# Kernel optimization log

Hardware: AMD Instinct MI355X
Metric: run time of the kernel (lower is better)

## Reference

```python
import jax, jax.numpy as jnp
import numpy as np

B, S, H = 1, 2048, 4096
NQ, NKV, D = 32, 8, 128
N_REP = NQ // NKV
SCALE = 1.0 / np.sqrt(D)
SOFTCAP = 30.0
EPS = 1e-5


def _rotate_half(x):
    x1, x2 = jnp.split(x, 2, axis=-1)
    return jnp.concatenate([-x2, x1], axis=-1)


def _rms_norm(x, w, eps=EPS):
    xf = x.astype(jnp.float32)
    norm = xf * jax.lax.rsqrt(jnp.mean(xf * xf, axis=-1, keepdims=True) + eps)
    return (w * norm).astype(x.dtype)


def setup_inputs() -> dict:
    key = jax.random.key(0)
    ks = jax.random.split(key, 8)
    hidden_states = jax.random.normal(ks[0], (B, S, H), dtype=jnp.float32)
    # causal additive mask
    causal = jnp.tril(jnp.ones((S, S), dtype=bool))
    attention_mask = jnp.where(causal, 0.0, -1e9)[None, None].astype(jnp.float32)
    # RoPE cache
    inv_freq = 1.0 / (10000.0 ** (np.arange(0, D, 2, dtype=np.float32) / D))
    t = np.arange(S, dtype=np.float32)
    freqs = np.outer(t, inv_freq)                      # (S, D/2)
    emb = np.concatenate([freqs, freqs], axis=-1)      # (S, D)
    cos = jnp.asarray(np.cos(emb))[None, None]         # (1,1,S,D)
    sin = jnp.asarray(np.sin(emb))[None, None]
    # params
    std = 0.02
    wq = jax.random.normal(ks[1], (NQ * D, H), dtype=jnp.float32) * std
    wk = jax.random.normal(ks[2], (NKV * D, H), dtype=jnp.float32) * std
    wv = jax.random.normal(ks[3], (NKV * D, H), dtype=jnp.float32) * std
    wo = jax.random.normal(ks[4], (H, NQ * D), dtype=jnp.float32) * std
    pre_norm_w = jnp.ones((H,), dtype=jnp.float32)
    q_norm_w = jnp.ones((D,), dtype=jnp.float32)
    k_norm_w = jnp.ones((D,), dtype=jnp.float32)
    return {
        "hidden_states": hidden_states, "attention_mask": attention_mask,
        "cos": cos, "sin": sin, "pre_norm_w": pre_norm_w,
        "wq": wq, "wk": wk, "wv": wv, "wo": wo,
        "q_norm_w": q_norm_w, "k_norm_w": k_norm_w,
    }


def reference(hidden_states, attention_mask, cos, sin, pre_norm_w,
              wq, wk, wv, wo, q_norm_w, k_norm_w):
    residual = hidden_states
    h = _rms_norm(hidden_states, pre_norm_w)
    bsz, seq_len, _ = h.shape
    # projections -> (b, heads, s, d)
    q = jnp.einsum('bsh,eh->bse', h, wq).reshape(bsz, seq_len, NQ, D).transpose(0, 2, 1, 3)
    k = jnp.einsum('bsh,eh->bse', h, wk).reshape(bsz, seq_len, NKV, D).transpose(0, 2, 1, 3)
    v = jnp.einsum('bsh,eh->bse', h, wv).reshape(bsz, seq_len, NKV, D).transpose(0, 2, 1, 3)
    # QK RMSNorm over head_dim
    q = _rms_norm(q, q_norm_w)
    k = _rms_norm(k, k_norm_w)
    # RoPE (full head_dim)
    q = q * cos + _rotate_half(q) * sin
    k = k * cos + _rotate_half(k) * sin
    # GQA: repeat kv heads
    k_exp = jnp.repeat(k, N_REP, axis=1)  # (b, NQ, s, d)
    v_exp = jnp.repeat(v, N_REP, axis=1)
    scores = jnp.einsum('bhqd,bhkd->bhqk', q, k_exp) * SCALE
    scores = SOFTCAP * jnp.tanh(scores / SOFTCAP)
    scores = scores + attention_mask
    probs = jax.nn.softmax(scores.astype(jnp.float32), axis=-1).astype(q.dtype)
    attn = jnp.einsum('bhqk,bhkd->bhqd', probs, v_exp)
    attn = attn.transpose(0, 2, 1, 3).reshape(bsz, seq_len, NQ * D)
    out = jnp.einsum('bse,he->bsh', attn, wo)
    return residual + out
```

## Files before the change

kernel.cpp:

```cpp
#include <hip/hip_runtime.h>
#include <cstdint>

typedef __bf16 bf16;
typedef __bf16 bf16x8 __attribute__((ext_vector_type(8)));
typedef __bf16 bf16x4 __attribute__((ext_vector_type(4)));
typedef float  f32x4  __attribute__((ext_vector_type(4)));

#define SEQ  2048
#define HID  4096
#define DH   128
#define NQH  32
#define NKVH 8
#define RSCALE 0.08838834764831845f
#define SOFTCAP 30.0f
#define L2E 1.4426950408889634f

__device__ __forceinline__ void gl2lds16(const void* g, void* l) {
  __builtin_amdgcn_global_load_lds(
      (const __attribute__((address_space(1))) unsigned int*)g,
      (__attribute__((address_space(3))) unsigned int*)l, 16, 0, 0);
}

__global__ void cvt_kernel(const float* __restrict__ in, bf16* __restrict__ out, int n4) {
  const int stride = gridDim.x * blockDim.x;
  for (int i = blockIdx.x * blockDim.x + threadIdx.x; i < n4; i += stride) {
    const float4 v = ((const float4*)in)[i];
    bf16x4 o = { (bf16)v.x, (bf16)v.y, (bf16)v.z, (bf16)v.w };
    *(bf16x4*)(out + (size_t)i * 4) = o;
  }
}

__global__ void rmsnorm_kernel(const float* __restrict__ x, const float* __restrict__ w,
                               bf16* __restrict__ out) {
  const int s = blockIdx.x;
  const float* xr = x + (size_t)s * HID;
  float4 v[4];
  float ss = 0.f;
#pragma unroll
  for (int j = 0; j < 4; ++j) {
    v[j] = ((const float4*)xr)[threadIdx.x + j * 256];
    ss += v[j].x * v[j].x + v[j].y * v[j].y + v[j].z * v[j].z + v[j].w * v[j].w;
  }
#pragma unroll
  for (int m = 1; m < 64; m <<= 1) ss += __shfl_xor(ss, m);
  __shared__ float red[4];
  if ((threadIdx.x & 63) == 0) red[threadIdx.x >> 6] = ss;
  __syncthreads();
  const float rn = rsqrtf((red[0] + red[1] + red[2] + red[3]) * (1.f / HID) + 1e-5f);
  bf16* orow = out + (size_t)s * HID;
#pragma unroll
  for (int j = 0; j < 4; ++j) {
    const int idx = (threadIdx.x + j * 256) * 4;
    const float4 wv = ((const float4*)w)[threadIdx.x + j * 256];
    bf16x4 o = { (bf16)(v[j].x * rn * wv.x), (bf16)(v[j].y * rn * wv.y),
                 (bf16)(v[j].z * rn * wv.z), (bf16)(v[j].w * rn * wv.w) };
    *(bf16x4*)(orow + idx) = o;
  }
}

template<bool FINAL>
__global__ __launch_bounds__(256, 3)
void gemm_bt(const bf16* __restrict__ A, const bf16* __restrict__ B,
             bf16* __restrict__ Cb, float* __restrict__ Cf,
             const float* __restrict__ resid, int M, int N, int K)
{
  __shared__ bf16 As[128 * 64];
  __shared__ bf16 Bs[128 * 64];
  const int tid  = threadIdx.x;
  const int lane = tid & 63;
  const int wave = tid >> 6;
  const int wm = wave >> 1, wn = wave & 1;

  const int gx = gridDim.x;
  const int nwg = gx * gridDim.y;
  int lin = blockIdx.x + gx * blockIdx.y;
  lin = (lin & 7) * (nwg >> 3) + (lin >> 3);
  const int m0 = (lin / gx) * 128, n0 = (lin % gx) * 128;

  f32x4 acc[4][4] = {};

  for (int kt = 0; kt < K; kt += 64) {
#pragma unroll
    for (int i = 0; i < 4; ++i) {
      const int c = wave * 4 + i;
      const int row = c * 8 + (lane >> 3);
      const int col8 = (lane & 7) ^ (row & 7);
      gl2lds16(A + (size_t)(m0 + row) * K + kt + col8 * 8, As + c * 512);
      gl2lds16(B + (size_t)(n0 + row) * K + kt + col8 * 8, Bs + c * 512);
    }
    __syncthreads();
#pragma unroll
    for (int ks = 0; ks < 2; ++ks) {
      bf16x8 af[4], bfv[4];
#pragma unroll
      for (int mi = 0; mi < 4; ++mi) {
        const int row = wm * 64 + mi * 16 + (lane & 15);
        const int slot = (ks * 4 + (lane >> 4)) ^ (row & 7);
        af[mi] = *(const bf16x8*)(As + row * 64 + slot * 8);
      }
#pragma unroll
      for (int ni = 0; ni < 4; ++ni) {
        const int row = wn * 64 + ni * 16 + (lane & 15);
        const int slot = (ks * 4 + (lane >> 4)) ^ (row & 7);
        bfv[ni] = *(const bf16x8*)(Bs + row * 64 + slot * 8);
      }
#pragma unroll
      for (int mi = 0; mi < 4; ++mi)
#pragma unroll
        for (int ni = 0; ni < 4; ++ni)
          acc[mi][ni] = __builtin_amdgcn_mfma_f32_16x16x32_bf16(af[mi], bfv[ni], acc[mi][ni], 0, 0, 0);
    }
    __syncthreads();
  }

#pragma unroll
  for (int mi = 0; mi < 4; ++mi) {
#pragma unroll
    for (int i = 0; i < 4; ++i) {
      const int m = m0 + wm * 64 + mi * 16 + (lane >> 4) * 4 + i;
#pragma unroll
      for (int ni = 0; ni < 4; ++ni) {
        const int n = n0 + wn * 64 + ni * 16 + (lane & 15);
        const float v = acc[mi][ni][i];
        if constexpr (FINAL) {
          Cf[(size_t)m * N + n] = v + resid[(size_t)m * N + n];
        } else {
          Cb[(size_t)m * N + n] = (bf16)v;
        }
      }
    }
  }
}

__global__ void qkrope_kernel(const bf16* __restrict__ qpj, const bf16* __restrict__ kpj,
                              const float* __restrict__ qw, const float* __restrict__ kw,
                              const float* __restrict__ cs, const float* __restrict__ sn,
                              bf16* __restrict__ qr, bf16* __restrict__ kr)
{
  const int w = blockIdx.x * 4 + (threadIdx.x >> 6);
  const int lane = threadIdx.x & 63;
  const int s = w / (NQH + NKVH);
  const int hh = w % (NQH + NKVH);
  const bf16* src; bf16* dst; const float* nw;
  if (hh < NQH) {
    src = qpj + (size_t)s * (NQH * DH) + hh * DH;
    dst = qr + ((size_t)hh * SEQ + s) * DH;
    nw = qw;
  } else {
    const int h2 = hh - NQH;
    src = kpj + (size_t)s * 2048 + h2 * DH;
    dst = kr + ((size_t)h2 * SEQ + s) * DH;
    nw = kw;
  }
  const float x0 = (float)src[lane], x1 = (float)src[lane + 64];
  float ss = x0 * x0 + x1 * x1;
#pragma unroll
  for (int m = 1; m < 64; m <<= 1) ss += __shfl_xor(ss, m);
  const float rn = rsqrtf(ss * (1.f / DH) + 1e-5f);
  const float n0 = x0 * rn * nw[lane], n1 = x1 * rn * nw[lane + 64];
  const float c0 = cs[s * DH + lane],      s0 = sn[s * DH + lane];
  const float c1 = cs[s * DH + lane + 64], s1 = sn[s * DH + lane + 64];
  dst[lane]      = (bf16)(n0 * c0 - n1 * s0);
  dst[lane + 64] = (bf16)(n1 * c1 + n0 * s1);
}

__global__ void vtrans_kernel(const bf16* __restrict__ vsrc, bf16* __restrict__ vt)
{
  __shared__ bf16 tbuf[64][33];
  const int s0 = blockIdx.x * 64;
  const int d0 = blockIdx.y * 32;
  const int h  = blockIdx.z;
  const int tid = threadIdx.x;
  {
    const int col = tid & 31, r0 = tid >> 5;
    for (int r = r0; r < 64; r += 8)
      tbuf[r][col] = vsrc[(size_t)(s0 + r) * 2048 + 1024 + h * DH + d0 + col];
  }
  __syncthreads();
  {
    const int sc = tid & 63, dr0 = tid >> 6;
    for (int d = dr0; d < 32; d += 4)
      vt[((size_t)h * DH + d0 + d) * SEQ + s0 + sc] = tbuf[sc][d];
  }
}

__global__ __launch_bounds__(256, 2)
void attn_kernel(const bf16* __restrict__ Q, const bf16* __restrict__ Kr,
                 const bf16* __restrict__ Vt, bf16* __restrict__ Oa)
{
  __shared__ bf16 Ks[2][64 * 128];
  __shared__ bf16 Vs[2][128 * 64];
  __shared__ bf16 Ps[4][32 * 64];

  const int tid = threadIdx.x, lane = tid & 63, wave = tid >> 6;

  const int lin  = blockIdx.x + 16 * blockIdx.y;
  const int slot = lin >> 8, idx = lin & 255;
  const int bx   = slot ? (15 - (idx & 15)) : (idx & 15);
  const int head = (slot << 4) | (idx >> 4);
  const int kvh  = head >> 2;
  const int q0   = bx * 128;
  const int wq0  = q0 + wave * 32;

  const bf16* Qh = Q  + (size_t)head * SEQ * DH;
  const bf16* Kh = Kr + (size_t)kvh * SEQ * DH;
  const bf16* Vh = Vt + (size_t)kvh * DH * SEQ;

  bf16x8 qf[2][4];
#pragma unroll
  for (int mt = 0; mt < 2; ++mt)
#pragma unroll
    for (int kc = 0; kc < 4; ++kc) {
      const int r = wq0 + mt * 16 + (lane & 15);
      qf[mt][kc] = *(const bf16x8*)(Qh + (size_t)r * DH + kc * 32 + (lane >> 4) * 8);
    }

  float lsum[2][4] = {};
  f32x4 o_acc[2][8] = {};

  const int ntiles = q0 / 64 + 2;

  auto stage = [&](int t, int b) {
    const int kv0 = t * 64;
    bf16* Kd = &Ks[b][0];
    bf16* Vd = &Vs[b][0];
#pragma unroll
    for (int i2 = 0; i2 < 4; ++i2) {
      const int c = wave * 4 + i2;
      {
        const int row = c * 4 + (lane >> 4);
        const int col8 = (lane & 15) ^ (row & 15);
        gl2lds16(Kh + (size_t)(kv0 + row) * DH + col8 * 8, Kd + c * 512);
      }
      {
        const int row = c * 8 + (lane >> 3);
        const int col8 = (lane & 7) ^ (row & 7);
        gl2lds16(Vh + (size_t)row * SEQ + kv0 + col8 * 8, Vd + c * 512);
      }
    }
  };

  stage(0, 0);
  __syncthreads();

  const float ZS = RSCALE / SOFTCAP;
  const float A1 = RSCALE * L2E;
  const float B3 = -(ZS * ZS) * (1.f / 3.f);
  const float B5 = (2.f / 15.f) * (ZS * ZS) * (ZS * ZS);
  const float C  = SOFTCAP * L2E;

  for (int t = 0; t < ntiles; ++t) {
    const int cur = t & 1;
    if (t + 1 < ntiles) stage(t + 1, cur ^ 1);
    const int kv0 = t * 64;
    const bf16* Kb = &Ks[cur][0];
    const bf16* Vb = &Vs[cur][0];

    if (kv0 <= wq0 + 31) {
      f32x4 sc[2][4] = {};
      __builtin_amdgcn_s_setprio(1);
#pragma unroll
      for (int ks = 0; ks < 4; ++ks) {
        bf16x8 kf[4];
#pragma unroll
        for (int nt = 0; nt < 4; ++nt) {
          const int row = nt * 16 + (lane & 15);
          const int sl = (ks * 4 + (lane >> 4)) ^ (row & 15);
          kf[nt] = *(const bf16x8*)(Kb + row * 128 + sl * 8);
        }
#pragma unroll
        for (int mt = 0; mt < 2; ++mt)
#pragma unroll
          for (int nt = 0; nt < 4; ++nt)
            sc[mt][nt] = __builtin_amdgcn_mfma_f32_16x16x32_bf16(qf[mt][ks], kf[nt], sc[mt][nt], 0, 0, 0);
      }
      __builtin_amdgcn_s_setprio(0);

      if (kv0 + 63 <= wq0) {
#pragma unroll
        for (int mt = 0; mt < 2; ++mt)
#pragma unroll
          for (int i = 0; i < 4; ++i)
#pragma unroll
            for (int nt = 0; nt < 4; ++nt) {
              const float s = sc[mt][nt][i];
              const float w = s * s;
              const float poly = fmaf(fmaf(B5, w, B3), w, 1.f);
              const float p = __builtin_amdgcn_exp2f(fmaf(s * poly, A1, -C));
              sc[mt][nt][i] = p;
              lsum[mt][i] += p;
            }
      } else {
#pragma unroll
        for (int mt = 0; mt < 2; ++mt)
#pragma unroll
          for (int i = 0; i < 4; ++i) {
            const int qrow = wq0 + mt * 16 + (lane >> 4) * 4 + i;
#pragma unroll
            for (int nt = 0; nt < 4; ++nt) {
              const int col = kv0 + nt * 16 + (lane & 15);
              const float s = sc[mt][nt][i];
              const float w = s * s;
              const float poly = fmaf(fmaf(B5, w, B3), w, 1.f);
              float p = __builtin_amdgcn_exp2f(fmaf(s * poly, A1, -C));
              if (col > qrow) p = 0.f;
              sc[mt][nt][i] = p;
              lsum[mt][i] += p;
            }
          }
      }

#pragma unroll
      for (int mt = 0; mt < 2; ++mt)
#pragma unroll
        for (int nt = 0; nt < 4; ++nt)
#pragma unroll
          for (int i = 0; i < 4; ++i) {
            const int r = mt * 16 + (lane >> 4) * 4 + i;
            const int colb = nt * 16 + (lane & 15);
            const int sl = (colb >> 3) ^ (r & 7);
            Ps[wave][r * 64 + sl * 8 + (colb & 7)] = (bf16)sc[mt][nt][i];
          }
      asm volatile("s_waitcnt lgkmcnt(0)" ::: "memory");
      __builtin_amdgcn_sched_barrier(0);

      __builtin_amdgcn_s_setprio(1);
#pragma unroll
      for (int ks2 = 0; ks2 < 2; ++ks2) {
        bf16x8 pf[2];
#pragma unroll
        for (int mt = 0; mt < 2; ++mt) {
          const int r = mt * 16 + (lane & 15);
          const int sl = (ks2 * 4 + (lane >> 4)) ^ (r & 7);
          pf[mt] = *(const bf16x8*)(&Ps[wave][r * 64 + sl * 8]);
        }
#pragma unroll
        for (int nt = 0; nt < 8; ++nt) {
          const int row = nt * 16 + (lane & 15);
          const int sl = (ks2 * 4 + (lane >> 4)) ^ (row & 7);
          const bf16x8 vf = *(const bf16x8*)(Vb + row * 64 + sl * 8);
          o_acc[0][nt] = __builtin_amdgcn_mfma_f32_16x16x32_bf16(pf[0], vf, o_acc[0][nt], 0, 0, 0);
          o_acc[1][nt] = __builtin_amdgcn_mfma_f32_16x16x32_bf16(pf[1], vf, o_acc[1][nt], 0, 0, 0);
        }
      }
      __builtin_amdgcn_s_setprio(0);
    }
    __syncthreads();
  }

#pragma unroll
  for (int mt = 0; mt < 2; ++mt)
#pragma unroll
    for (int i = 0; i < 4; ++i) {
      float l = lsum[mt][i];
#pragma unroll
      for (int m = 1; m < 16; m <<= 1) l += __shfl_xor(l, m);
      const int qrow = wq0 + mt * 16 + (lane >> 4) * 4 + i;
      const float inv_l = 1.f / l;
#pragma unroll
      for (int nt = 0; nt < 8; ++nt) {
        const int d = nt * 16 + (lane & 15);
        Oa[(size_t)qrow * HID + head * DH + d] = (bf16)(o_acc[mt][nt][i] * inv_l);
      }
    }
}

extern "C" void kernel_launch(void* const* d_in, const int* in_sizes, int n_in,
                              void* d_out, int out_size, void* d_ws, size_t ws_size,
                              hipStream_t stream)
{
  const float* hidden = (const float*)d_in[0];
  const float* cosb   = (const float*)d_in[2];
  const float* sinb   = (const float*)d_in[3];
  const float* prew   = (const float*)d_in[4];
  const float* wq     = (const float*)d_in[5];
  const float* wk     = (const float*)d_in[6];
  const float* wv     = (const float*)d_in[7];
  const float* wo     = (const float*)d_in[8];
  const float* qnw    = (const float*)d_in[9];
  const float* knw    = (const float*)d_in[10];
  float* outp = (float*)d_out;
  char* ws = (char*)d_ws;

  bf16* wqb  = (bf16*)(ws + 0);
  bf16* wkvb = (bf16*)(ws + 33554432);
  bf16* kvpj = (bf16*)(ws + 50331648);
  bf16* hb   = (bf16*)(ws + 58720256);
  bf16* qpj  = (bf16*)(ws + 75497472);
  bf16* kr   = (bf16*)(ws + 92274688);
  bf16* vt   = (bf16*)(ws + 96468992);

  cvt_kernel<<<2048, 256, 0, stream>>>(wq, wqb, (NQH * DH) * HID / 4);
  cvt_kernel<<<1024, 256, 0, stream>>>(wk, wkvb, (NKVH * DH) * HID / 4);
  cvt_kernel<<<1024, 256, 0, stream>>>(wv, wkvb + (size_t)(NKVH * DH) * HID, (NKVH * DH) * HID / 4);
  rmsnorm_kernel<<<SEQ, 256, 0, stream>>>(hidden, prew, hb);

  gemm_bt<false><<<dim3(32, 16), 256, 0, stream>>>(hb, wqb,  qpj,  nullptr, nullptr, SEQ, 4096, 4096);
  gemm_bt<false><<<dim3(16, 16), 256, 0, stream>>>(hb, wkvb, kvpj, nullptr, nullptr, SEQ, 2048, 4096);

  qkrope_kernel<<<SEQ * (NQH + NKVH) / 4, 256, 0, stream>>>(qpj, kvpj, qnw, knw, cosb, sinb, hb, kr);
  vtrans_kernel<<<dim3(32, 4, 8), 256, 0, stream>>>(kvpj, vt);
  cvt_kernel<<<2048, 256, 0, stream>>>(wo, wqb, (NQH * DH) * HID / 4);

  attn_kernel<<<dim3(16, 32), 256, 0, stream>>>(hb, kr, vt, qpj);

  gemm_bt<true><<<dim3(32, 16), 256, 0, stream>>>(qpj, wqb, nullptr, outp, hidden, SEQ, 4096, 4096);
}
```

Baseline: 376.2 us.

## Fuse QKV projection GEMMs and add triple-buffered 8-wave 128x256 GEMM pipeline

Merges the Q and KV projection weights into one contiguous QKV matrix so a single GEMM produces all projections, and retargets the rope and V-transpose kernels to the fused layout. Replaces the 4-wave 128x128 GEMM with an 8-wave 128x256 tile kernel that uses 144KB of dynamic LDS for triple buffering. Loads are prefetched two tiles ahead, split across the two k-substeps, with explicit waitcnt, barriers and setprio around the MFMAs. The goal is to overlap global loads with compute and cut launch and tail overhead. In exchange it runs only one workgroup per CU and depends on fragile hand-placed synchronisation.

```diff
diff --git a/kernel.cpp b/kernel.cpp
--- a/kernel.cpp
+++ b/kernel.cpp
@@ -11,6 +11,7 @@
 #define DH   128
 #define NQH  32
 #define NKVH 8
+#define NTOT 6144
 #define RSCALE 0.08838834764831845f
 #define SOFTCAP 30.0f
 #define L2E 1.4426950408889634f
@@ -59,36 +60,68 @@
 }
 
 template<bool FINAL>
-__global__ __launch_bounds__(256, 3)
-void gemm_bt(const bf16* __restrict__ A, const bf16* __restrict__ B,
-             bf16* __restrict__ Cb, float* __restrict__ Cf,
-             const float* __restrict__ resid, int M, int N, int K)
+__global__ __launch_bounds__(512, 1)
+void gemm8(const bf16* __restrict__ A, const bf16* __restrict__ B,
+           bf16* __restrict__ Cb, float* __restrict__ Cf,
+           const float* __restrict__ resid, int M, int N, int K)
 {
-  __shared__ bf16 As[128 * 64];
-  __shared__ bf16 Bs[128 * 64];
+  extern __shared__ char smem[];
   const int tid  = threadIdx.x;
   const int lane = tid & 63;
   const int wave = tid >> 6;
-  const int wm = wave >> 1, wn = wave & 1;
+  const int wm = wave >> 2, wn = wave & 3;
 
   const int gx = gridDim.x;
   const int nwg = gx * gridDim.y;
   int lin = blockIdx.x + gx * blockIdx.y;
   lin = (lin & 7) * (nwg >> 3) + (lin >> 3);
-  const int m0 = (lin / gx) * 128, n0 = (lin % gx) * 128;
+  const int m0 = (lin / gx) * 128;
+  const int n0 = (lin % gx) * 256;
+
+  auto Abuf = [&](int b) -> bf16* { return (bf16*)(smem + b * 49152); };
+  auto Bbuf = [&](int b) -> bf16* { return (bf16*)(smem + b * 49152 + 16384); };
+
+  auto stage_half = [&](int kt, int b, int h) {
+    if (h == 0) {
+#pragma unroll
+      for (int i = 0; i < 2; ++i) {
+        const int c = wave * 2 + i;
+        const int row = c * 8 + (lane >> 3);
+        const int col8 = (lane & 7) ^ (row & 7);
+        gl2lds16(A + (size_t)(m0 + row) * K + kt + col8 * 8, Abuf(b) + c * 512);
+      }
+      {
+        const int c = wave * 4;
+        const int row = c * 8 + (lane >> 3);
+        const int col8 = (lane & 7) ^ (row & 7);
+        gl2lds16(B + (size_t)(n0 + row) * K + kt + col8 * 8, Bbuf(b) + c * 512);
+      }
+    } else {
+#pragma unroll
+      for (int i = 1; i < 4; ++i) {
+        const int c = wave * 4 + i;
+        const int row = c * 8 + (lane >> 3);
+        const int col8 = (lane & 7) ^ (row & 7);
+        gl2lds16(B + (size_t)(n0 + row) * K + kt + col8 * 8, Bbuf(b) + c * 512);
+      }
+    }
+  };
 
   f32x4 acc[4][4] = {};
-
-  for (int kt = 0; kt < K; kt += 64) {
-#pragma unroll
-    for (int i = 0; i < 4; ++i) {
-      const int c = wave * 4 + i;
-      const int row = c * 8 + (lane >> 3);
-      const int col8 = (lane & 7) ^ (row & 7);
-      gl2lds16(A + (size_t)(m0 + row) * K + kt + col8 * 8, As + c * 512);
-      gl2lds16(B + (size_t)(n0 + row) * K + kt + col8 * 8, Bs + c * 512);
-    }
-    __syncthreads();
+  const int nt = K / 64;
+
+  stage_half(0, 0, 0);  stage_half(0, 0, 1);
+  stage_half(64, 1, 0); stage_half(64, 1, 1);
+  asm volatile("s_waitcnt vmcnt(6)" ::: "memory");
+  __builtin_amdgcn_s_barrier();
+
+  for (int t = 0; t < nt; ++t) {
+    const int cur = t % 3;
+    const bf16* Ab = Abuf(cur);
+    const bf16* Bb = Bbuf(cur);
+    const int nxt = (t + 2) % 3;
+    const bool pf = (t + 2) < nt;
+
 #pragma unroll
     for (int ks = 0; ks < 2; ++ks) {
       bf16x8 af[4], bfv[4];
@@ -96,21 +129,33 @@
       for (int mi = 0; mi < 4; ++mi) {
         const int row = wm * 64 + mi * 16 + (lane & 15);
         const int slot = (ks * 4 + (lane >> 4)) ^ (row & 7);
-        af[mi] = *(const bf16x8*)(As + row * 64 + slot * 8);
+        af[mi] = *(const bf16x8*)(Ab + row * 64 + slot * 8);
       }
 #pragma unroll
       for (int ni = 0; ni < 4; ++ni) {
         const int row = wn * 64 + ni * 16 + (lane & 15);
         const int slot = (ks * 4 + (lane >> 4)) ^ (row & 7);
-        bfv[ni] = *(const bf16x8*)(Bs + row * 64 + slot * 8);
-      }
+        bfv[ni] = *(const bf16x8*)(Bb + row * 64 + slot * 8);
+      }
+      if (pf) stage_half((t + 2) * 64, nxt, ks);
+
+      __builtin_amdgcn_s_barrier();
+      asm volatile("s_waitcnt lgkmcnt(0)" ::: "memory");
+      __builtin_amdgcn_sched_barrier(0);
+      __builtin_amdgcn_s_setprio(1);
 #pragma unroll
       for (int mi = 0; mi < 4; ++mi)
 #pragma unroll
         for (int ni = 0; ni < 4; ++ni)
           acc[mi][ni] = __builtin_amdgcn_mfma_f32_16x16x32_bf16(af[mi], bfv[ni], acc[mi][ni], 0, 0, 0);
-    }
-    __syncthreads();
+      __builtin_amdgcn_s_setprio(0);
+
+      if (ks == 1) {
+        if (pf)                asm volatile("s_waitcnt vmcnt(6)" ::: "memory");
+        else if (t + 1 < nt)   asm volatile("s_waitcnt vmcnt(0)" ::: "memory");
+      }
+      __builtin_amdgcn_s_barrier();
+    }
   }
 
 #pragma unroll
@@ -132,7 +177,7 @@
   }
 }
 
-__global__ void qkrope_kernel(const bf16* __restrict__ qpj, const bf16* __restrict__ kpj,
+__global__ void qkrope_kernel(const bf16* __restrict__ qkv,
                               const float* __restrict__ qw, const float* __restrict__ kw,
                               const float* __restrict__ cs, const float* __restrict__ sn,
                               bf16* __restrict__ qr, bf16* __restrict__ kr)
@@ -143,12 +188,12 @@
   const int hh = w % (NQH + NKVH);
   const bf16* src; bf16* dst; const float* nw;
   if (hh < NQH) {
-    src = qpj + (size_t)s * (NQH * DH) + hh * DH;
+    src = qkv + (size_t)s * NTOT + hh * DH;
     dst = qr + ((size_t)hh * SEQ + s) * DH;
     nw = qw;
   } else {
     const int h2 = hh - NQH;
-    src = kpj + (size_t)s * 2048 + h2 * DH;
+    src = qkv + (size_t)s * NTOT + 4096 + h2 * DH;
     dst = kr + ((size_t)h2 * SEQ + s) * DH;
     nw = kw;
   }
@@ -164,7 +209,7 @@
   dst[lane + 64] = (bf16)(n1 * c1 + n0 * s1);
 }
 
-__global__ void vtrans_kernel(const bf16* __restrict__ vsrc, bf16* __restrict__ vt)
+__global__ void vtrans_kernel(const bf16* __restrict__ qkv, bf16* __restrict__ vt)
 {
   __shared__ bf16 tbuf[64][33];
   const int s0 = blockIdx.x * 64;
@@ -174,7 +219,7 @@
   {
     const int col = tid & 31, r0 = tid >> 5;
     for (int r = r0; r < 64; r += 8)
-      tbuf[r][col] = vsrc[(size_t)(s0 + r) * 2048 + 1024 + h * DH + d0 + col];
+      tbuf[r][col] = qkv[(size_t)(s0 + r) * NTOT + 5120 + h * DH + d0 + col];
   }
   __syncthreads();
   {
@@ -382,27 +427,28 @@
   float* outp = (float*)d_out;
   char* ws = (char*)d_ws;
 
-  bf16* wqb  = (bf16*)(ws + 0);
-  bf16* wkvb = (bf16*)(ws + 33554432);
-  bf16* kvpj = (bf16*)(ws + 50331648);
-  bf16* hb   = (bf16*)(ws + 58720256);
-  bf16* qpj  = (bf16*)(ws + 75497472);
+  bf16* wqkv = (bf16*)(ws + 0);
+  bf16* hb   = (bf16*)(ws + 50331648);
+  bf16* qkvp = (bf16*)(ws + 67108864);
   bf16* kr   = (bf16*)(ws + 92274688);
   bf16* vt   = (bf16*)(ws + 96468992);
-
-  cvt_kernel<<<2048, 256, 0, stream>>>(wq, wqb, (NQH * DH) * HID / 4);
-  cvt_kernel<<<1024, 256, 0, stream>>>(wk, wkvb, (NKVH * DH) * HID / 4);
-  cvt_kernel<<<1024, 256, 0, stream>>>(wv, wkvb + (size_t)(NKVH * DH) * HID, (NKVH * DH) * HID / 4);
+  bf16* wob  = wqkv;
+
+  cvt_kernel<<<2048, 256, 0, stream>>>(wq, wqkv, 4096 * HID / 4);
+  cvt_kernel<<<1024, 256, 0, stream>>>(wk, wqkv + (size_t)4096 * HID, 1024 * HID / 4);
+  cvt_kernel<<<1024, 256, 0, stream>>>(wv, wqkv + (size_t)5120 * HID, 1024 * HID / 4);
   rmsnorm_kernel<<<SEQ, 256, 0, stream>>>(hidden, prew, hb);
 
-  gemm_bt<false><<<dim3(32, 16), 256, 0, stream>>>(hb, wqb,  qpj,  nullptr, nullptr, SEQ, 4096, 4096);
-  gemm_bt<false><<<dim3(16, 16), 256, 0, stream>>>(hb, wkvb, kvpj, nullptr, nullptr, SEQ, 2048, 4096);
-
-  qkrope_kernel<<<SEQ * (NQH + NKVH) / 4, 256, 0, stream>>>(qpj, kvpj, qnw, knw, cosb, sinb, hb, kr);
-  vtrans_kernel<<<dim3(32, 4, 8), 256, 0, stream>>>(kvpj, vt);
-  cvt_kernel<<<2048, 256, 0, stream>>>(wo, wqb, (NQH * DH) * HID / 4);
-
-  attn_kernel<<<dim3(16, 32), 256, 0, stream>>>(hb, kr, vt, qpj);
-
-  gemm_bt<true><<<dim3(32, 16), 256, 0, stream>>>(qpj, wqb, nullptr, outp, hidden, SEQ, 4096, 4096);
-}
+  gemm8<false><<<dim3(NTOT / 256, SEQ / 128), 512, 147456, stream>>>(
+      hb, wqkv, qkvp, nullptr, nullptr, SEQ, NTOT, HID);
+
+  cvt_kernel<<<2048, 256, 0, stream>>>(wo, wob, HID * HID / 4);
+
+  qkrope_kernel<<<SEQ * (NQH + NKVH) / 4, 256, 0, stream>>>(qkvp, qnw, knw, cosb, sinb, hb, kr);
+  vtrans_kernel<<<dim3(32, 4, 8), 256, 0, stream>>>(qkvp, vt);
+
+  attn_kernel<<<dim3(16, 32), 256, 0, stream>>>(hb, kr, vt, qkvp);
+
+  gemm8<true><<<dim3(HID / 256, SEQ / 128), 512, 147456, stream>>>(
+      qkvp, wob, nullptr, outp, hidden, SEQ, HID, HID);
+}
```

Measured after the change: 373.6 us. No clear change (-0.7%).

## Fuse fp32-to-bf16 weight conversion into GEMM B loads and merge QKV projections

Applied to the files above, without the earlier changes.

Removes the standalone weight conversion kernels. The GEMM now reads fp32 weights directly, converts them to bf16 in registers and writes them into swizzled LDS. The Q, K and V projections are merged into one GEMM over a concatenated 6144-wide output, which selects the source weight per column tile. This saves the extra conversion passes and kernel launches, but every M-tile now re-reads fp32 weights through synchronous register loads, occupancy drops from 3 to 2 blocks, and the workgroup swizzle for L2 locality is removed.

```diff
diff --git a/kernel.cpp b/kernel.cpp
--- a/kernel.cpp
+++ b/kernel.cpp
@@ -11,6 +11,7 @@
 #define DH   128
 #define NQH  32
 #define NKVH 8
+#define NTOT 6144
 #define RSCALE 0.08838834764831845f
 #define SOFTCAP 30.0f
 #define L2E 1.4426950408889634f
@@ -19,15 +20,6 @@
   __builtin_amdgcn_global_load_lds(
       (const __attribute__((address_space(1))) unsigned int*)g,
       (__attribute__((address_space(3))) unsigned int*)l, 16, 0, 0);
-}
-
-__global__ void cvt_kernel(const float* __restrict__ in, bf16* __restrict__ out, int n4) {
-  const int stride = gridDim.x * blockDim.x;
-  for (int i = blockIdx.x * blockDim.x + threadIdx.x; i < n4; i += stride) {
-    const float4 v = ((const float4*)in)[i];
-    bf16x4 o = { (bf16)v.x, (bf16)v.y, (bf16)v.z, (bf16)v.w };
-    *(bf16x4*)(out + (size_t)i * 4) = o;
-  }
 }
 
 __global__ void rmsnorm_kernel(const float* __restrict__ x, const float* __restrict__ w,
@@ -59,8 +51,10 @@
 }
 
 template<bool FINAL>
-__global__ __launch_bounds__(256, 3)
-void gemm_bt(const bf16* __restrict__ A, const bf16* __restrict__ B,
+__global__ __launch_bounds__(256, 2)
+void gemm_fb(const bf16* __restrict__ A,
+             const float* __restrict__ Bq, const float* __restrict__ Bk,
+             const float* __restrict__ Bv,
              bf16* __restrict__ Cb, float* __restrict__ Cf,
              const float* __restrict__ resid, int M, int N, int K)
 {
@@ -70,25 +64,53 @@
   const int lane = tid & 63;
   const int wave = tid >> 6;
   const int wm = wave >> 1, wn = wave & 1;
-
-  const int gx = gridDim.x;
-  const int nwg = gx * gridDim.y;
-  int lin = blockIdx.x + gx * blockIdx.y;
-  lin = (lin & 7) * (nwg >> 3) + (lin >> 3);
-  const int m0 = (lin / gx) * 128, n0 = (lin % gx) * 128;
+  const int m0 = blockIdx.y * 128, n0 = blockIdx.x * 128;
+
+  const float* Bsrc; int nrow0;
+  if (n0 < 4096)      { Bsrc = Bq; nrow0 = n0; }
+  else if (n0 < 5120) { Bsrc = Bk; nrow0 = n0 - 4096; }
+  else                { Bsrc = Bv; nrow0 = n0 - 5120; }
+
+  const int brow = tid >> 1;
+  const int bcol = (tid & 1) * 32;
+  const float* brp = Bsrc + (size_t)(nrow0 + brow) * K + bcol;
 
   f32x4 acc[4][4] = {};
 
   for (int kt = 0; kt < K; kt += 64) {
+    float4 b0 = ((const float4*)(brp + kt))[0];
+    float4 b1 = ((const float4*)(brp + kt))[1];
+    float4 b2 = ((const float4*)(brp + kt))[2];
+    float4 b3 = ((const float4*)(brp + kt))[3];
+    float4 b4 = ((const float4*)(brp + kt))[4];
+    float4 b5 = ((const float4*)(brp + kt))[5];
+    float4 b6 = ((const float4*)(brp + kt))[6];
+    float4 b7 = ((const float4*)(brp + kt))[7];
 #pragma unroll
     for (int i = 0; i < 4; ++i) {
       const int c = wave * 4 + i;
       const int row = c * 8 + (lane >> 3);
       const int col8 = (lane & 7) ^ (row & 7);
       gl2lds16(A + (size_t)(m0 + row) * K + kt + col8 * 8, As + c * 512);
-      gl2lds16(B + (size_t)(n0 + row) * K + kt + col8 * 8, Bs + c * 512);
+    }
+    {
+      const int rb = brow * 64;
+      const int rx = brow & 7;
+      bf16x8 w0 = { (bf16)b0.x, (bf16)b0.y, (bf16)b0.z, (bf16)b0.w,
+                    (bf16)b1.x, (bf16)b1.y, (bf16)b1.z, (bf16)b1.w };
+      *(bf16x8*)(Bs + rb + (((bcol >> 3) + 0) ^ rx) * 8) = w0;
+      bf16x8 w1 = { (bf16)b2.x, (bf16)b2.y, (bf16)b2.z, (bf16)b2.w,
+                    (bf16)b3.x, (bf16)b3.y, (bf16)b3.z, (bf16)b3.w };
+      *(bf16x8*)(Bs + rb + (((bcol >> 3) + 1) ^ rx) * 8) = w1;
+      bf16x8 w2 = { (bf16)b4.x, (bf16)b4.y, (bf16)b4.z, (bf16)b4.w,
+                    (bf16)b5.x, (bf16)b5.y, (bf16)b5.z, (bf16)b5.w };
+      *(bf16x8*)(Bs + rb + (((bcol >> 3) + 2) ^ rx) * 8) = w2;
+      bf16x8 w3 = { (bf16)b6.x, (bf16)b6.y, (bf16)b6.z, (bf16)b6.w,
+                    (bf16)b7.x, (bf16)b7.y, (bf16)b7.z, (bf16)b7.w };
+      *(bf16x8*)(Bs + rb + (((bcol >> 3) + 3) ^ rx) * 8) = w3;
     }
     __syncthreads();
+
 #pragma unroll
     for (int ks = 0; ks < 2; ++ks) {
       bf16x8 af[4], bfv[4];
@@ -132,7 +154,7 @@
   }
 }
 
-__global__ void qkrope_kernel(const bf16* __restrict__ qpj, const bf16* __restrict__ kpj,
+__global__ void qkrope_kernel(const bf16* __restrict__ qkv,
                               const float* __restrict__ qw, const float* __restrict__ kw,
                               const float* __restrict__ cs, const float* __restrict__ sn,
                               bf16* __restrict__ qr, bf16* __restrict__ kr)
@@ -143,12 +165,12 @@
   const int hh = w % (NQH + NKVH);
   const bf16* src; bf16* dst; const float* nw;
   if (hh < NQH) {
-    src = qpj + (size_t)s * (NQH * DH) + hh * DH;
+    src = qkv + (size_t)s * NTOT + hh * DH;
     dst = qr + ((size_t)hh * SEQ + s) * DH;
     nw = qw;
   } else {
     const int h2 = hh - NQH;
-    src = kpj + (size_t)s * 2048 + h2 * DH;
+    src = qkv + (size_t)s * NTOT + 4096 + h2 * DH;
     dst = kr + ((size_t)h2 * SEQ + s) * DH;
     nw = kw;
   }
@@ -164,7 +186,7 @@
   dst[lane + 64] = (bf16)(n1 * c1 + n0 * s1);
 }
 
-__global__ void vtrans_kernel(const bf16* __restrict__ vsrc, bf16* __restrict__ vt)
+__global__ void vtrans_kernel(const bf16* __restrict__ qkv, bf16* __restrict__ vt)
 {
   __shared__ bf16 tbuf[64][33];
   const int s0 = blockIdx.x * 64;
@@ -174,7 +196,7 @@
   {
     const int col = tid & 31, r0 = tid >> 5;
     for (int r = r0; r < 64; r += 8)
-      tbuf[r][col] = vsrc[(size_t)(s0 + r) * 2048 + 1024 + h * DH + d0 + col];
+      tbuf[r][col] = qkv[(size_t)(s0 + r) * NTOT + 5120 + h * DH + d0 + col];
   }
   __syncthreads();
   {
@@ -382,27 +404,21 @@
   float* outp = (float*)d_out;
   char* ws = (char*)d_ws;
 
-  bf16* wqb  = (bf16*)(ws + 0);
-  bf16* wkvb = (bf16*)(ws + 33554432);
-  bf16* kvpj = (bf16*)(ws + 50331648);
-  bf16* hb   = (bf16*)(ws + 58720256);
-  bf16* qpj  = (bf16*)(ws + 75497472);
-  bf16* kr   = (bf16*)(ws + 92274688);
-  bf16* vt   = (bf16*)(ws + 96468992);
-
-  cvt_kernel<<<2048, 256, 0, stream>>>(wq, wqb, (NQH * DH) * HID / 4);
-  cvt_kernel<<<1024, 256, 0, stream>>>(wk, wkvb, (NKVH * DH) * HID / 4);
-  cvt_kernel<<<1024, 256, 0, stream>>>(wv, wkvb + (size_t)(NKVH * DH) * HID, (NKVH * DH) * HID / 4);
+  bf16* hb   = (bf16*)(ws + 0);
+  bf16* qkvp = (bf16*)(ws + 16777216);
+  bf16* kr   = (bf16*)(ws + 41943040);
+  bf16* vt   = (bf16*)(ws + 46137344);
+
   rmsnorm_kernel<<<SEQ, 256, 0, stream>>>(hidden, prew, hb);
 
-  gemm_bt<false><<<dim3(32, 16), 256, 0, stream>>>(hb, wqb,  qpj,  nullptr, nullptr, SEQ, 4096, 4096);
-  gemm_bt<false><<<dim3(16, 16), 256, 0, stream>>>(hb, wkvb, kvpj, nullptr, nullptr, SEQ, 2048, 4096);
-
-  qkrope_kernel<<<SEQ * (NQH + NKVH) / 4, 256, 0, stream>>>(qpj, kvpj, qnw, knw, cosb, sinb, hb, kr);
-  vtrans_kernel<<<dim3(32, 4, 8), 256, 0, stream>>>(kvpj, vt);
-  cvt_kernel<<<2048, 256, 0, stream>>>(wo, wqb, (NQH * DH) * HID / 4);
-
-  attn_kernel<<<dim3(16, 32), 256, 0, stream>>>(hb, kr, vt, qpj);
-
-  gemm_bt<true><<<dim3(32, 16), 256, 0, stream>>>(qpj, wqb, nullptr, outp, hidden, SEQ, 4096, 4096);
-}
+  gemm_fb<false><<<dim3(NTOT / 128, SEQ / 128), 256, 0, stream>>>(
+      hb, wq, wk, wv, qkvp, nullptr, nullptr, SEQ, NTOT, HID);
+
+  qkrope_kernel<<<SEQ * (NQH + NKVH) / 4, 256, 0, stream>>>(qkvp, qnw, knw, cosb, sinb, hb, kr);
+  vtrans_kernel<<<dim3(32, 4, 8), 256, 0, stream>>>(qkvp, vt);
+
+  attn_kernel<<<dim3(16, 32), 256, 0, stream>>>(hb, kr, vt, qkvp);
+
+  gemm_fb<true><<<dim3(HID / 128, SEQ / 128), 256, 0, stream>>>(
+      qkvp, wo, wo, wo, nullptr, outp, hidden, SEQ, HID, HID);
+}
```

New measurement: 507.4 us. 1.35x slower.
